# Performance work log

Measured on AMD Instinct MI355X. Metric: run time of the kernel, lower is better.

## Reference

```python
import jax, jax.numpy as jnp
import numpy as np

ALPHA = 32.0
RANK = 16
SCALE = ALPHA / RANK


def setup_inputs() -> dict:
    key = jax.random.key(0)
    k1, k2, k3, k4, k5 = jax.random.split(key, 5)
    B, S, D_IN, D_OUT, N = 4, 2048, 4096, 4096, 8
    x = jax.random.normal(k1, (B, S, D_IN), dtype=jnp.float32)
    routing_w = jax.random.uniform(k2, (B, N), dtype=jnp.float32)
    W_base = jax.random.normal(k3, (D_OUT, D_IN), dtype=jnp.float32) * 0.02
    lora_down = jax.random.normal(k4, (N, RANK, D_IN), dtype=jnp.float32) * 0.02
    lora_up = jax.random.normal(k5, (N, D_OUT, RANK), dtype=jnp.float32) * 0.02
    return {"x": x, "routing_w": routing_w, "W_base": W_base,
            "lora_down": lora_down, "lora_up": lora_up}


def reference(x, routing_w, W_base, lora_down, lora_up):
    # base linear: [B,S,D_in] @ [D_out,D_in]^T -> [B,S,D_out]
    base_out = jnp.einsum('bsi,oi->bso', x, W_base)
    # per-expert LoRA down-proj: [B,S,D_in] x [N,R,D_in] -> [B,N,S,R]
    down = jnp.einsum('bsi,nri->bnsr', x, lora_down)
    # up-proj + scale: [B,N,S,R] x [N,D_out,R] -> [B,N,S,D_out]
    up = jnp.einsum('bnsr,nor->bnso', down, lora_up) * SCALE
    # routing-weighted sum over experts: [B,N] x [B,N,S,D_out] -> [B,S,D_out]
    adapter_out = jnp.einsum('bn,bnso->bso', routing_w, up)
    return base_out + adapter_out
```

## Files before the change

kernel.cpp:

```cpp
#include <hip/hip_runtime.h>
#include <hip/hip_bf16.h>
#include <stdint.h>

#define TOK    8192
#define DIN    4096
#define DOUT   4096
#define NEXP   8
#define RK     16
#define NRANK  128
#define KE     4224
#define SEQB   2048
#define LSCALE 2.0f
#define KSPLIT 16
#define KSLICE (DIN / KSPLIT)

typedef __attribute__((ext_vector_type(8))) short bf8_t;
typedef __attribute__((ext_vector_type(4))) float f4_t;

__device__ __forceinline__ void async_copy16(const void* g, void* l) {
  __builtin_amdgcn_global_load_lds((const __attribute__((address_space(1))) void*)g,
                                   (__attribute__((address_space(3))) void*)l,
                                   16, 0, 0);
}

__device__ __forceinline__ ushort f2bf(float f) {
  __hip_bfloat16 h = __float2bfloat16(f);
  return *reinterpret_cast<ushort*>(&h);
}

#define R0 (TOK * DIN / 8)
#define R1 (DOUT * DIN / 8)
#define R2 (DOUT * NEXP * 2)
#define R3 (NRANK * DIN / 8)
#define RTOT (R0 + R1 + R2 + R3)

__global__ __launch_bounds__(256)
void cvt_all_kernel(const float* __restrict__ x, const float* __restrict__ wb,
                    const float* __restrict__ lu, const float* __restrict__ ld,
                    ushort* __restrict__ Xe, ushort* __restrict__ Wc,
                    ushort* __restrict__ Ldb) {
  int i = blockIdx.x * 256 + threadIdx.x;
  const float* src;
  ushort* dst;
  if (i < R0) {
    int t = i >> 9;
    int c = (i & 511) * 8;
    src = x + (size_t)t * DIN + c;
    dst = Xe + (size_t)t * KE + c;
  } else if (i < R0 + R1) {
    int j = i - R0;
    int t = j >> 9;
    int c = (j & 511) * 8;
    src = wb + (size_t)t * DIN + c;
    dst = Wc + (size_t)t * KE + c;
  } else if (i < R0 + R1 + R2) {
    int j = i - (R0 + R1);
    int o = j >> 4;
    int rem = j & 15;
    int n = rem >> 1;
    int half = rem & 1;
    src = lu + ((size_t)n * DOUT + o) * RK + half * 8;
    dst = Wc + (size_t)o * KE + DIN + n * RK + half * 8;
  } else {
    int j = i - (R0 + R1 + R2);
    src = ld + (size_t)j * 8;
    dst = Ldb + (size_t)j * 8;
  }
  const float4* s = reinterpret_cast<const float4*>(src);
  float4 a = s[0], b = s[1];
  union { ushort u[8]; uint4 v; } o;
  o.u[0]=f2bf(a.x); o.u[1]=f2bf(a.y); o.u[2]=f2bf(a.z); o.u[3]=f2bf(a.w);
  o.u[4]=f2bf(b.x); o.u[5]=f2bf(b.y); o.u[6]=f2bf(b.z); o.u[7]=f2bf(b.w);
  *reinterpret_cast<uint4*>(dst) = o.v;
}

__global__ __launch_bounds__(256)
void down_k16_kernel(const ushort* __restrict__ A,
                     const ushort* __restrict__ Bm,
                     float* __restrict__ D32,
                     ushort* __restrict__ Xe,
                     const float* __restrict__ rw,
                     unsigned int* __restrict__ cnt) {
  __shared__ __align__(16) ushort As[128 * 32];
  __shared__ __align__(16) ushort Bs[128 * 32];

  const int tid  = threadIdx.x;
  const int wave = tid >> 6;
  const int lane = tid & 63;
  const int bm   = blockIdx.y * 128;
  const int wm = wave & 1, wn = wave >> 1;

  f4_t acc[4][4];
#pragma unroll
  for (int i = 0; i < 4; i++)
#pragma unroll
    for (int j = 0; j < 4; j++) acc[i][j] = (f4_t){0.f, 0.f, 0.f, 0.f};

  const int f0 = tid * 8;
  const int r0 = f0 >> 5, c0 = f0 & 31;
  const int f1 = (256 + tid) * 8;
  const int r1 = f1 >> 5, c1 = f1 & 31;
  const int l0 = (wave << 6) * 8;
  const int l1 = (256 + (wave << 6)) * 8;

  const ushort* Ar = As + (wm * 64 + (lane & 15)) * 32 + (lane >> 4) * 8;
  const ushort* Br = Bs + (wn * 64 + (lane & 15)) * 32 + (lane >> 4) * 8;

  const int kbase = blockIdx.z * KSLICE;
  const int kend  = kbase + KSLICE;

  for (int k0 = kbase; k0 < kend; k0 += 32) {
    __syncthreads();
    async_copy16(A  + (size_t)(bm + r0) * KE  + k0 + c0, (void*)(As + l0));
    async_copy16(A  + (size_t)(bm + r1) * KE  + k0 + c1, (void*)(As + l1));
    async_copy16(Bm + (size_t)r0 * DIN + k0 + c0, (void*)(Bs + l0));
    async_copy16(Bm + (size_t)r1 * DIN + k0 + c1, (void*)(Bs + l1));
    __syncthreads();
    bf8_t av[4], bv[4];
#pragma unroll
    for (int i = 0; i < 4; i++) av[i] = *(const bf8_t*)(Ar + i * 16 * 32);
#pragma unroll
    for (int j = 0; j < 4; j++) bv[j] = *(const bf8_t*)(Br + j * 16 * 32);
#pragma unroll
    for (int i = 0; i < 4; i++)
#pragma unroll
      for (int j = 0; j < 4; j++)
        acc[i][j] = __builtin_amdgcn_mfma_f32_16x16x32_bf16(av[i], bv[j], acc[i][j], 0, 0, 0);
  }

#pragma unroll
  for (int i = 0; i < 4; i++) {
    int row = bm + wm * 64 + i * 16 + (lane >> 4) * 4;
#pragma unroll
    for (int j = 0; j < 4; j++) {
      int col = wn * 64 + j * 16 + (lane & 15);
#pragma unroll
      for (int rr = 0; rr < 4; rr++)
        atomicAdd(&D32[(size_t)(row + rr) * NRANK + col], acc[i][j][rr]);
    }
  }

  __threadfence();
  __syncthreads();
  __shared__ int last_s;
  if (tid == 0)
    last_s = (atomicAdd(&cnt[blockIdx.y], 1u) == KSPLIT - 1);
  __syncthreads();
  if (!last_s) return;
  __threadfence();

  for (int it = tid; it < 128 * 32; it += 256) {
    int t = bm + (it >> 5);
    int g = (it & 31) * 4;
    float4 a = *reinterpret_cast<const float4*>(D32 + (size_t)t * NRANK + g);
    int n = g >> 4;
    int bb = t / SEQB;
    float s = rw[bb * NEXP + n] * LSCALE;
    union { ushort u[4]; uint2 v; } o;
    o.u[0] = f2bf(a.x * s);
    o.u[1] = f2bf(a.y * s);
    o.u[2] = f2bf(a.z * s);
    o.u[3] = f2bf(a.w * s);
    *reinterpret_cast<uint2*>(Xe + (size_t)t * KE + DIN + g) = o.v;
  }
}

#define BK32  32
#define NT132 (KE / BK32)

__global__ __launch_bounds__(512, 2)
void gemm256(const ushort* __restrict__ A, const ushort* __restrict__ Bm,
             float* __restrict__ C) {
  __shared__ __align__(16) ushort As[4][256 * 32];
  __shared__ __align__(16) ushort Bs[4][256 * 32];

  const int tid  = threadIdx.x;
  const int w    = tid >> 6;
  const int lane = tid & 63;
  const int wm   = w >> 2;
  const int wn   = w & 3;

  const int bid = blockIdx.x;
  const int xg  = bid & 7;
  const int jj  = bid >> 3;
  const int bm  = (((xg & 3) << 3) + (jj & 7)) << 8;
  const int bn  = (((xg >> 2) << 3) + (jj >> 3)) << 8;

  f4_t acc[8][4];
#pragma unroll
  for (int i = 0; i < 8; ++i)
#pragma unroll
    for (int q = 0; q < 4; ++q) acc[i][q] = (f4_t){0.f, 0.f, 0.f, 0.f};

  const int frow = lane & 15;
  const int cbs  = (((lane >> 4) ^ (frow >> 1)) << 4);
  const int ar0  = wm * 128;
  const int br0  = wn * 64;

  const int sxr = (lane >> 3) << 4;
  const int t0  = (w << 10) + (lane << 4);
  const int l0b = t0 ^ sxr;
  const int l1b = (t0 + 8192) ^ sxr;
  const size_t goff0 = (size_t)(l0b >> 6) * KE + ((l0b & 63) >> 1);
  const size_t goff1 = (size_t)(l1b >> 6) * KE + ((l1b & 63) >> 1);
  const int ld0 = (w << 9);
  const int ld1 = (w << 9) + 4096;

  const ushort* Ap = A  + (size_t)bm * KE;
  const ushort* Bp = Bm + (size_t)bn * KE;

#define STAGE_A256(kt, buf) do {                                   \
    const ushort* cp_ = Ap + (size_t)(kt) * BK32;                  \
    async_copy16(cp_ + goff0, (void*)(As[buf] + ld0));             \
    async_copy16(cp_ + goff1, (void*)(As[buf] + ld1));             \
  } while (0)
#define STAGE_B256(kt, buf) do {                                   \
    const ushort* cp_ = Bp + (size_t)(kt) * BK32;                  \
    async_copy16(cp_ + goff0, (void*)(Bs[buf] + ld0));             \
    async_copy16(cp_ + goff1, (void*)(Bs[buf] + ld1));             \
  } while (0)
#define RD_A(s_, mh, f_) (*(const bf8_t*)((const char*)As[s_] + \
    (((ar0 + (mh) * 64 + (f_) * 16 + frow) << 6) ^ cbs)))
#define RD_B(s_, g_) (*(const bf8_t*)((const char*)Bs[s_] + \
    (((br0 + (g_) * 16 + frow) << 6) ^ cbs)))

  STAGE_A256(0, 0); STAGE_B256(0, 0);
  STAGE_A256(1, 1); STAGE_B256(1, 1);
  STAGE_A256(2, 2); STAGE_B256(2, 2);
  asm volatile("s_waitcnt vmcnt(4)" ::: "memory");
  __builtin_amdgcn_s_barrier();

  bf8_t fA0[2][4], fA1[2][4], fB[2][4];
#pragma unroll
  for (int f = 0; f < 4; ++f) fA0[0][f] = RD_A(0, 0, f);
#pragma unroll
  for (int g = 0; g < 4; ++g) fB[0][g]  = RD_B(0, g);

  for (int t2 = 0; t2 < NT132; t2 += 2) {
#pragma unroll
    for (int u = 0; u < 2; ++u) {
      const int T  = t2 + u;
      const int b  = T & 3;
      const int b1 = (T + 1) & 3;
      const int sb = (T + 3) & 3;

      __builtin_amdgcn_s_setprio(1);
#pragma unroll
      for (int f = 0; f < 4; ++f) fA1[u][f] = RD_A(b, 1, f);
      if (T + 3 < NT132) STAGE_A256(T + 3, sb);
#pragma unroll
      for (int f = 0; f < 4; ++f)
#pragma unroll
        for (int g = 0; g < 4; ++g)
          acc[f][g] = __builtin_amdgcn_mfma_f32_16x16x32_bf16(fA0[u][f], fB[u][g], acc[f][g], 0, 0, 0);
      __builtin_amdgcn_s_setprio(0);
      __builtin_amdgcn_s_barrier();

      __builtin_amdgcn_s_setprio(1);
      if (T + 1 < NT132) {
#pragma unroll
        for (int f = 0; f < 4; ++f) fA0[u ^ 1][f] = RD_A(b1, 0, f);
#pragma unroll
        for (int g = 0; g < 4; ++g) fB[u ^ 1][g]  = RD_B(b1, g);
      }
      if (T + 3 < NT132) STAGE_B256(T + 3, sb);
#pragma unroll
      for (int f = 0; f < 4; ++f)
#pragma unroll
        for (int g = 0; g < 4; ++g)
          acc[4 + f][g] = __builtin_amdgcn_mfma_f32_16x16x32_bf16(fA1[u][f], fB[u][g], acc[4 + f][g], 0, 0, 0);
      __builtin_amdgcn_s_setprio(0);
      if (T < NT132 - 4) asm volatile("s_waitcnt vmcnt(4)" ::: "memory");
      else               asm volatile("s_waitcnt vmcnt(0)" ::: "memory");
      __builtin_amdgcn_s_barrier();
    }
  }

#pragma unroll
  for (int i = 0; i < 8; ++i) {
    int row = bm + wm * 128 + i * 16 + (lane >> 4) * 4;
#pragma unroll
    for (int q = 0; q < 4; ++q) {
      int col = bn + wn * 64 + q * 16 + (lane & 15);
#pragma unroll
      for (int rr = 0; rr < 4; ++rr)
        C[(size_t)(row + rr) * DOUT + col] = acc[i][q][rr];
    }
  }
#undef STAGE_A256
#undef STAGE_B256
#undef RD_A
#undef RD_B
}

extern "C" void kernel_launch(void* const* d_in, const int* in_sizes, int n_in,
                              void* d_out, int out_size, void* d_ws, size_t ws_size,
                              hipStream_t stream) {
  const float* x  = (const float*)d_in[0];
  const float* rw = (const float*)d_in[1];
  const float* wb = (const float*)d_in[2];
  const float* ld = (const float*)d_in[3];
  const float* lu = (const float*)d_in[4];
  float* out = (float*)d_out;

  ushort* Xe  = (ushort*)d_ws;
  ushort* Wc  = Xe + (size_t)TOK * KE;
  ushort* Ldb = Wc + (size_t)DOUT * KE;
  float*  D32 = (float*)(Ldb + (size_t)NRANK * DIN);
  unsigned int* cnt = (unsigned int*)(D32 + (size_t)TOK * NRANK);

  hipMemsetAsync(D32, 0, (size_t)TOK * NRANK * sizeof(float), stream);
  hipMemsetAsync(cnt, 0, (TOK / 128) * sizeof(unsigned int), stream);

  cvt_all_kernel<<<RTOT / 256, 256, 0, stream>>>(x, wb, lu, ld, Xe, Wc, Ldb);

  down_k16_kernel<<<dim3(1, TOK / 128, KSPLIT), 256, 0, stream>>>(
      Xe, Ldb, D32, Xe, rw, cnt);

  gemm256<<<dim3((TOK / 256) * (DOUT / 256)), 512, 0, stream>>>(Xe, Wc, out);
}
```

Baseline: 682.2 us.

## Replace atomic split-K reduction in down-projection with per-split partial buffers

The LoRA down-projection kernel moves from 128-row tiles split 16 ways along K, with float atomics into one shared buffer, to 64-row tiles split 4 ways. Each split now writes plain stores into its own partial buffer, and the last-arriving block sums the four partials before scaling and converting to bf16. This removes the per-element atomic traffic and the memset that zeroed the accumulator buffer. In exchange it uses a larger workspace for the four partial buffers and runs fewer K-splits per tile, which lowers K-parallelism in this kernel.

```diff
diff --git a/kernel.cpp b/kernel.cpp
--- a/kernel.cpp
+++ b/kernel.cpp
@@ -11,7 +11,7 @@
 #define KE     4224
 #define SEQB   2048
 #define LSCALE 2.0f
-#define KSPLIT 16
+#define KSPLIT 4
 #define KSLICE (DIN / KSPLIT)
 
 typedef __attribute__((ext_vector_type(8))) short bf8_t;
@@ -75,24 +75,25 @@
 }
 
 __global__ __launch_bounds__(256)
-void down_k16_kernel(const ushort* __restrict__ A,
-                     const ushort* __restrict__ Bm,
-                     float* __restrict__ D32,
-                     ushort* __restrict__ Xe,
-                     const float* __restrict__ rw,
-                     unsigned int* __restrict__ cnt) {
-  __shared__ __align__(16) ushort As[128 * 32];
+void down64_kernel(const ushort* __restrict__ A,
+                   const ushort* __restrict__ Bm,
+                   float* __restrict__ D32,
+                   ushort* __restrict__ Xe,
+                   const float* __restrict__ rw,
+                   unsigned int* __restrict__ cnt) {
+  __shared__ __align__(16) ushort As[64 * 32];
   __shared__ __align__(16) ushort Bs[128 * 32];
 
   const int tid  = threadIdx.x;
   const int wave = tid >> 6;
   const int lane = tid & 63;
-  const int bm   = blockIdx.y * 128;
+  const int bm   = blockIdx.y * 64;
+  const int z    = blockIdx.z;
   const int wm = wave & 1, wn = wave >> 1;
 
-  f4_t acc[4][4];
-#pragma unroll
-  for (int i = 0; i < 4; i++)
+  f4_t acc[2][4];
+#pragma unroll
+  for (int i = 0; i < 2; i++)
 #pragma unroll
     for (int j = 0; j < 4; j++) acc[i][j] = (f4_t){0.f, 0.f, 0.f, 0.f};
 
@@ -103,40 +104,38 @@
   const int l0 = (wave << 6) * 8;
   const int l1 = (256 + (wave << 6)) * 8;
 
-  const ushort* Ar = As + (wm * 64 + (lane & 15)) * 32 + (lane >> 4) * 8;
+  const ushort* Ar = As + (wm * 32 + (lane & 15)) * 32 + (lane >> 4) * 8;
   const ushort* Br = Bs + (wn * 64 + (lane & 15)) * 32 + (lane >> 4) * 8;
 
-  const int kbase = blockIdx.z * KSLICE;
-  const int kend  = kbase + KSLICE;
-
-  for (int k0 = kbase; k0 < kend; k0 += 32) {
+  const int kbase = z * KSLICE;
+  for (int k0 = kbase; k0 < kbase + KSLICE; k0 += 32) {
     __syncthreads();
     async_copy16(A  + (size_t)(bm + r0) * KE  + k0 + c0, (void*)(As + l0));
-    async_copy16(A  + (size_t)(bm + r1) * KE  + k0 + c1, (void*)(As + l1));
-    async_copy16(Bm + (size_t)r0 * DIN + k0 + c0, (void*)(Bs + l0));
-    async_copy16(Bm + (size_t)r1 * DIN + k0 + c1, (void*)(Bs + l1));
+    async_copy16(Bm + (size_t)r0 * DIN + k0 + c0,        (void*)(Bs + l0));
+    async_copy16(Bm + (size_t)r1 * DIN + k0 + c1,        (void*)(Bs + l1));
     __syncthreads();
-    bf8_t av[4], bv[4];
-#pragma unroll
-    for (int i = 0; i < 4; i++) av[i] = *(const bf8_t*)(Ar + i * 16 * 32);
+    bf8_t av[2], bv[4];
+#pragma unroll
+    for (int i = 0; i < 2; i++) av[i] = *(const bf8_t*)(Ar + i * 16 * 32);
 #pragma unroll
     for (int j = 0; j < 4; j++) bv[j] = *(const bf8_t*)(Br + j * 16 * 32);
 #pragma unroll
-    for (int i = 0; i < 4; i++)
+    for (int i = 0; i < 2; i++)
 #pragma unroll
       for (int j = 0; j < 4; j++)
         acc[i][j] = __builtin_amdgcn_mfma_f32_16x16x32_bf16(av[i], bv[j], acc[i][j], 0, 0, 0);
   }
 
-#pragma unroll
-  for (int i = 0; i < 4; i++) {
-    int row = bm + wm * 64 + i * 16 + (lane >> 4) * 4;
+  float* Dz = D32 + (size_t)z * TOK * NRANK;
+#pragma unroll
+  for (int i = 0; i < 2; i++) {
+    int row = bm + wm * 32 + i * 16 + (lane >> 4) * 4;
 #pragma unroll
     for (int j = 0; j < 4; j++) {
       int col = wn * 64 + j * 16 + (lane & 15);
 #pragma unroll
       for (int rr = 0; rr < 4; rr++)
-        atomicAdd(&D32[(size_t)(row + rr) * NRANK + col], acc[i][j][rr]);
+        Dz[(size_t)(row + rr) * NRANK + col] = acc[i][j][rr];
     }
   }
 
@@ -149,18 +148,23 @@
   if (!last_s) return;
   __threadfence();
 
-  for (int it = tid; it < 128 * 32; it += 256) {
+  const size_t ss = (size_t)TOK * NRANK;
+  for (int it = tid; it < 64 * 32; it += 256) {
     int t = bm + (it >> 5);
     int g = (it & 31) * 4;
-    float4 a = *reinterpret_cast<const float4*>(D32 + (size_t)t * NRANK + g);
+    size_t base = (size_t)t * NRANK + g;
+    float4 a = *reinterpret_cast<const float4*>(D32 + base);
+    float4 b = *reinterpret_cast<const float4*>(D32 + ss + base);
+    float4 c = *reinterpret_cast<const float4*>(D32 + 2 * ss + base);
+    float4 d = *reinterpret_cast<const float4*>(D32 + 3 * ss + base);
     int n = g >> 4;
     int bb = t / SEQB;
     float s = rw[bb * NEXP + n] * LSCALE;
     union { ushort u[4]; uint2 v; } o;
-    o.u[0] = f2bf(a.x * s);
-    o.u[1] = f2bf(a.y * s);
-    o.u[2] = f2bf(a.z * s);
-    o.u[3] = f2bf(a.w * s);
+    o.u[0] = f2bf((a.x + b.x + c.x + d.x) * s);
+    o.u[1] = f2bf((a.y + b.y + c.y + d.y) * s);
+    o.u[2] = f2bf((a.z + b.z + c.z + d.z) * s);
+    o.u[3] = f2bf((a.w + b.w + c.w + d.w) * s);
     *reinterpret_cast<uint2*>(Xe + (size_t)t * KE + DIN + g) = o.v;
   }
 }
@@ -307,14 +311,13 @@
   ushort* Wc  = Xe + (size_t)TOK * KE;
   ushort* Ldb = Wc + (size_t)DOUT * KE;
   float*  D32 = (float*)(Ldb + (size_t)NRANK * DIN);
-  unsigned int* cnt = (unsigned int*)(D32 + (size_t)TOK * NRANK);
-
-  hipMemsetAsync(D32, 0, (size_t)TOK * NRANK * sizeof(float), stream);
-  hipMemsetAsync(cnt, 0, (TOK / 128) * sizeof(unsigned int), stream);
+  unsigned int* cnt = (unsigned int*)(D32 + (size_t)KSPLIT * TOK * NRANK);
+
+  hipMemsetAsync(cnt, 0, (TOK / 64) * sizeof(unsigned int), stream);
 
   cvt_all_kernel<<<RTOT / 256, 256, 0, stream>>>(x, wb, lu, ld, Xe, Wc, Ldb);
 
-  down_k16_kernel<<<dim3(1, TOK / 128, KSPLIT), 256, 0, stream>>>(
+  down64_kernel<<<dim3(1, TOK / 64, KSPLIT), 256, 0, stream>>>(
       Xe, Ldb, D32, Xe, rw, cnt);
 
   gemm256<<<dim3((TOK / 256) * (DOUT / 256)), 512, 0, stream>>>(Xe, Wc, out);
```

After: 641.8 us. 1.06x faster.
